# Optimization experiments

Hardware: AMD Instinct MI355X
Metric: run time of the kernel (lower is better)

The kernel has to match this reference:

```python
import jax, jax.numpy as jnp
from jax import lax
import numpy as np

B, K, H, W = 16, 8, 256, 256


def setup_inputs() -> dict:
    key = jax.random.key(0)
    masks = jax.random.normal(key, (B, K, H, W), dtype=jnp.float32)
    return {"masks": masks}


def _nlccs_loss_one(mask):
    """Per-mask loss. mask: (H, W) float, already rescaled/clamped.

    Replicates cv2.connectedComponentsWithStats (8-connectivity, background is
    a single label regardless of connectivity), sorts components by area, and
    suppresses (zeroes a pmask over) the bounding box of the second-largest
    component, then returns mean(pmask * mask).
    """
    h, w = mask.shape
    S = h * w  # sentinel / background label
    sent = jnp.int32(S)
    fg = lax.stop_gradient(mask) > 0.5  # cv2 threshold (arr > 0.5)
    idx = jnp.arange(S, dtype=jnp.int32).reshape(h, w)
    lab0 = jnp.where(fg, idx, sent)

    def step(lab):
        # 8-connectivity neighbor-min propagation (cv2 default connectivity=8)
        p = jnp.pad(lab, 1, constant_values=S)
        m = lab
        for dy in (-1, 0, 1):
            for dx in (-1, 0, 1):
                if dy == 0 and dx == 0:
                    continue
                m = jnp.minimum(m, p[1 + dy:1 + dy + h, 1 + dx:1 + dx + w])
        lab = jnp.where(fg, m, sent)
        # pointer jumping: lab <- lab[lab] for log-time convergence
        ext = jnp.concatenate([lab.reshape(-1), jnp.array([S], jnp.int32)])
        return jnp.where(fg, ext[lab], sent)

    def cond(c):
        lab, prev = c
        return jnp.any(lab != prev)

    def body(c):
        lab, _ = c
        return step(lab), lab

    lab, _ = lax.while_loop(cond, body, (step(lab0), lab0))

    # per-label areas; background pixels all share label S (like cv2 label 0)
    areas = jnp.zeros(S + 1, jnp.int32).at[lab.reshape(-1)].add(1)
    _, top_idx = lax.top_k(areas, 2)
    second = top_idx[1]  # stats sorted by area -> stats[-2]

    # bounding box of the second-largest component
    sel = lab == second
    rows = jnp.arange(h, dtype=jnp.int32)[:, None]
    cols = jnp.arange(w, dtype=jnp.int32)[None, :]
    h0 = jnp.min(jnp.where(sel, rows, h))
    h1 = jnp.max(jnp.where(sel, rows, -1)) + 1
    w0 = jnp.min(jnp.where(sel, cols, w))
    w1 = jnp.max(jnp.where(sel, cols, -1)) + 1
    inside = (rows >= h0) & (rows < h1) & (cols >= w0) & (cols < w1)
    pmask = 1.0 - inside.astype(mask.dtype)  # pmask[h0:h1, w0:w1] = 0
    return (pmask * mask).mean()


def reference(masks):
    # masks: (b, k, h, w)
    m = jnp.maximum((masks + 1.0) * 0.5, 0.0)  # ((masks+1)/2).clamp(min=0)
    flat = m.reshape(-1, m.shape[-2], m.shape[-1])  # (b*k, h, w)
    losses = jax.vmap(_nlccs_loss_one)(flat)
    return losses.mean()
```

## Files before the change

kernel.cpp:

```cpp
#include <hip/hip_runtime.h>

#define HH 256
#define WW 256
#define SS 65536
#define NM 128
#define TRR 16
#define NT2 16
#define RMX 2048
#define SPT 1024
#define SPM 16384

struct Meta {
  double dsum[NM];
  int h0[NM]; int h1[NM]; int w0[NM]; int w1[NM];
};

__device__ __forceinline__ int find_c(int* L, int x) {
  int p = L[x];
  if (p == x) return x;
  int root = p, q = L[root];
  while (q != root) { root = q; q = L[root]; }
  if (root != p) L[x] = root;
  return root;
}

__device__ void unite(int* L, int a, int b) {
  bool done = false;
  do {
    a = find_c(L, a);
    b = find_c(L, b);
    if (a < b)      { int old = atomicMin(&L[b], a); done = (old == b); b = old; }
    else if (b < a) { int old = atomicMin(&L[a], b); done = (old == a); a = old; }
    else done = true;
  } while (!done);
}

__device__ __forceinline__ int find_halve(int* L, int x) {
  int p = L[x];
  while (p != x) {
    int gp = L[p];
    if (gp == p) return p;
    L[x] = gp;
    x = p; p = gp;
  }
  return x;
}

__device__ __forceinline__ int cid(const unsigned long long* rm,
                                   const int* rpre, int r) {
  int w = r >> 6, b = r & 63;
  return rpre[w] + (int)__popcll(rm[w] & (b ? ((1ull << b) - 1) : 0ull));
}

__device__ __forceinline__ unsigned long long mask_le(int b) {
  return (b == 63) ? ~0ull : ((1ull << (b + 1)) - 1);
}
__device__ __forceinline__ unsigned long long mask_lt(int b) {
  return b ? ((1ull << b) - 1) : 0ull;
}

__global__ __launch_bounds__(512)
void k_local(const float* __restrict__ in, int cb,
             int* __restrict__ gp, int* __restrict__ ga,
             unsigned int* __restrict__ gbb, unsigned short* __restrict__ gl,
             unsigned short* __restrict__ gbrow, int* __restrict__ gnr,
             double* __restrict__ tdsum, unsigned int* __restrict__ tbb,
             int* __restrict__ gfg0) {
  __shared__ unsigned long long sfgw[TRR][4];
  __shared__ unsigned char sfgc[TRR][32];
  __shared__ unsigned long long srs[TRR][4];
  __shared__ int wpre64[64];
  __shared__ int snr;
  __shared__ int sspan[RMX];
  __shared__ int suf[RMX];
  __shared__ unsigned long long rootm[32];
  __shared__ int rpre[32];
  __shared__ int sA[SPT], sW0[SPT], sW1[SPT], sH0[SPT], sH1[SPT];
  __shared__ double sred[8];
  __shared__ int sbb[4][8];

  int q = blockIdx.x, lm = q >> 4, tile = q & 15;
  int tid = threadIdx.x, lane = tid & 63, wv = tid >> 6;
  int gm = cb + lm, R0 = tile << 4;

  int r1 = tid >> 5, cs = tid & 31;
  const float4* src =
      (const float4*)(in + ((size_t)gm << 16) + ((R0 + r1) << 8) + (cs << 3));
  double dsum = 0.0;
  unsigned int fgb = 0;
  for (int k = 0; k < 2; k++) {
    float4 v = src[k];
    float m0 = fmaxf((v.x + 1.0f) * 0.5f, 0.0f);
    float m1 = fmaxf((v.y + 1.0f) * 0.5f, 0.0f);
    float m2 = fmaxf((v.z + 1.0f) * 0.5f, 0.0f);
    float m3 = fmaxf((v.w + 1.0f) * 0.5f, 0.0f);
    dsum += (double)m0 + (double)m1 + (double)m2 + (double)m3;
    fgb |= ((m0 > 0.5f) ? 1u : 0u) << (4 * k);
    fgb |= ((m1 > 0.5f) ? 1u : 0u) << (4 * k + 1);
    fgb |= ((m2 > 0.5f) ? 1u : 0u) << (4 * k + 2);
    fgb |= ((m3 > 0.5f) ? 1u : 0u) << (4 * k + 3);
  }
  sfgc[r1][cs] = (unsigned char)fgb;
  __syncthreads();
  if (tid < 64) {
    int row = tid >> 2, w = tid & 3;
    const unsigned char* pc = &sfgc[row][w << 3];
    unsigned long long wd = 0;
    for (int i = 0; i < 8; i++) wd |= ((unsigned long long)pc[i]) << (i << 3);
    sfgw[row][w] = wd;
  }
  __syncthreads();

  if (tid < 64) {
    int row = tid >> 2, w = tid & 3;
    unsigned long long W = sfgw[row][w];
    unsigned long long carry = (w > 0) ? (sfgw[row][w - 1] >> 63) : 0ull;
    unsigned long long rs = W & ~((W << 1) | carry);
    srs[row][w] = rs;
    int cnt = (int)__popcll(rs);
    int sa = cnt;
    for (int off = 1; off < 64; off <<= 1) {
      int t = __shfl_up(sa, off);
      if (tid >= off) sa += t;
    }
    wpre64[tid] = sa - cnt;
    if (tid == 63) snr = sa;
    int id = sa - cnt;
    unsigned long long bits = rs;
    while (bits) {
      int a = (int)__ffsll(bits) - 1;
      bits &= bits - 1;
      int A = (w << 6) + a;
      unsigned long long inv = ~(W >> a);
      int len = inv ? ((int)__ffsll(inv) - 1) : (64 - a);
      if (len == 64 - a) {
        for (int w2 = w + 1; w2 < 4; w2++) {
          unsigned long long iv2 = ~sfgw[row][w2];
          int t = iv2 ? ((int)__ffsll(iv2) - 1) : 64;
          len += t;
          if (t < 64) break;
        }
      }
      sspan[id] = (row << 16) | (A << 8) | (A + len - 1);
      suf[id] = id;
      id++;
    }
  } else {
    for (int s = tid - 64; s < SPT; s += 448) {
      sA[s] = 0; sW0[s] = WW; sW1[s] = -1; sH0[s] = TRR; sH1[s] = -1;
    }
  }
  __syncthreads();

  int nr = snr;

  for (int i = tid; i < nr; i += 512) {
    int sp = sspan[i];
    int row = sp >> 16, a = (sp >> 8) & 255, b = sp & 255;
    if (row == 0) continue;
    int lo = max(a - 1, 0), hi = min(b + 1, 255);
    const unsigned long long* Wp = sfgw[row - 1];
    const unsigned long long* Rp = srs[row - 1];
    int prebase = (row - 1) << 2;
    int lw = lo >> 6, lb = lo & 63;
    if (((Wp[lw] >> lb) & 1) && !((Rp[lw] >> lb) & 1)) {
      int j = wpre64[prebase + lw] + (int)__popcll(Rp[lw] & mask_le(lb)) - 1;
      unite(suf, i, j);
    }
    for (int w = lw; w <= (hi >> 6); w++) {
      unsigned long long m = Rp[w];
      if (w == lw) m &= ~mask_lt(lb);
      if (w == (hi >> 6)) m &= mask_le(hi & 63);
      int base2 = wpre64[prebase + w];
      while (m) {
        int bb = (int)__ffsll(m) - 1;
        m &= m - 1;
        int j = base2 + (int)__popcll(Rp[w] & mask_lt(bb));
        unite(suf, i, j);
      }
    }
  }
  __syncthreads();

  for (int j = 0; j < 4; j++) {
    int i = tid + (j << 9);
    unsigned long long bal = __ballot(i < nr && suf[i] == i);
    if (lane == 0) rootm[wv + (j << 3)] = bal;
  }
  __syncthreads();
  if (tid < 32) {
    int pc = (int)__popcll(rootm[tid]);
    int sa = pc;
    for (int off = 1; off < 32; off <<= 1) {
      int t = __shfl_up(sa, off);
      if (tid >= off) sa += t;
    }
    rpre[tid] = sa - pc;
  }
  __syncthreads();

  for (int i = tid; i < nr; i += 512) {
    int root = find_halve(suf, i);
    int id = cid(rootm, rpre, root);
    int sp = sspan[i];
    int row = sp >> 16, a = (sp >> 8) & 255, b = sp & 255;
    atomicAdd(&sA[id], b - a + 1);
    if (a < sW0[id]) atomicMin(&sW0[id], a);
    if (b > sW1[id]) atomicMax(&sW1[id], b);
    if (row < sH0[id]) atomicMin(&sH0[id], row);
    if (row > sH1[id]) atomicMax(&sH1[id], row);
  }
  __syncthreads();

  int nc = rpre[31] + (int)__popcll(rootm[31]);
  for (int i = tid; i < nr; i += 512) {
    if (suf[i] == i) {
      int id = cid(rootm, rpre, i);
      int gid = (lm << 14) + (tile << 10) + id;
      int sp = sspan[i];
      gp[gid] = gid;
      ga[gid] = sA[id];
      gl[gid] = (unsigned short)((tile << 12) + ((sp >> 16) << 8) +
                                 ((sp >> 8) & 255));
      gbb[gid] = ((unsigned)(R0 + sH0[id]) << 24) | ((unsigned)sW0[id] << 16)
               | ((unsigned)(R0 + sH1[id]) << 8) | (unsigned)sW1[id];
    }
  }
  {
    int c = tid & 255, topbot = tid >> 8;
    int brow = topbot ? (TRR - 1) : 0;
    unsigned short val = 0xFFFF;
    if ((sfgw[brow][c >> 6] >> (c & 63)) & 1) {
      int w = c >> 6, bb = c & 63;
      int id = wpre64[(brow << 2) + w] +
               (int)__popcll(srs[brow][w] & mask_le(bb)) - 1;
      int root = find_halve(suf, id);
      val = (unsigned short)((tile << 10) + cid(rootm, rpre, root));
    }
    gbrow[(q << 9) + (topbot ? 256 : 0) + c] = val;
  }
  if (tid == 0) gnr[q] = nc;

  int c = tid & 255, half = (tid >> 8) << 3;
  int bh0r = TRR, bh1r = -1;
  bool anybg = false;
  for (int row = half; row < half + 8; row++) {
    if (!((sfgw[row][c >> 6] >> (c & 63)) & 1)) {
      anybg = true;
      bh0r = min(bh0r, row); bh1r = max(bh1r, row);
    }
  }
  int bw0r = anybg ? c : WW, bw1r = anybg ? c : -1;
  for (int off = 32; off > 0; off >>= 1) {
    bw0r = min(bw0r, __shfl_down(bw0r, off));
    bw1r = max(bw1r, __shfl_down(bw1r, off));
    bh0r = min(bh0r, __shfl_down(bh0r, off));
    bh1r = max(bh1r, __shfl_down(bh1r, off));
  }
  if (lane == 0) { sbb[0][wv] = bw0r; sbb[1][wv] = bw1r;
                   sbb[2][wv] = bh0r; sbb[3][wv] = bh1r; }
  for (int off = 32; off > 0; off >>= 1) dsum += __shfl_down(dsum, off);
  if (lane == 0) sred[wv] = dsum;
  __syncthreads();
  if (tid == 0) {
    int a0 = sbb[0][0], a1 = sbb[1][0], a2 = sbb[2][0], a3 = sbb[3][0];
    for (int i = 1; i < 8; i++) {
      a0 = min(a0, sbb[0][i]); a1 = max(a1, sbb[1][i]);
      a2 = min(a2, sbb[2][i]); a3 = max(a3, sbb[3][i]);
    }
    unsigned pack = (a1 >= 0)
        ? (((unsigned)(R0 + a2) << 24) | ((unsigned)a0 << 16) |
           ((unsigned)(R0 + a3) << 8) | (unsigned)a1)
        : 0xFFFF0000u;
    tbb[q] = pack;
    double t = 0.0;
    for (int i = 0; i < 8; i++) t += sred[i];
    tdsum[q] = t;
    if (tile == 0) gfg0[lm] = (int)(sfgw[0][0] & 1ull);
  }
}

__global__ void k_seam(int* __restrict__ gp,
                       const unsigned short* __restrict__ gbrow) {
  int b = blockIdx.x;
  int lm = b / 15, s = b % 15;
  int tb = lm << 4;
  int sbase = lm << 14;
  const unsigned short* up = gbrow + ((tb + s) << 9) + 256;
  const unsigned short* lo = gbrow + ((tb + s + 1) << 9);
  int c = threadIdx.x;
  unsigned short v16 = lo[c];
  if (v16 == 0xFFFF) return;
  int v = sbase + v16;
  bool wfg = (c > 0) && (lo[c - 1] != 0xFFFF);
  unsigned short n16 = up[c];
  if (!wfg) {
    if (n16 != 0xFFFF) unite(gp, v, sbase + n16);
    else if (c > 0 && up[c - 1] != 0xFFFF) unite(gp, v, sbase + up[c - 1]);
  }
  if (n16 == 0xFFFF && c < 255 && up[c + 1] != 0xFFFF)
    unite(gp, v, sbase + up[c + 1]);
}

__global__ void k_push(int* __restrict__ gp, int* __restrict__ ga,
                       unsigned int* __restrict__ gbb,
                       const int* __restrict__ gnr) {
  int q = blockIdx.x;
  int lm = q >> 4;
  int sbase = lm << 14;
  int nc = gnr[q];
  int tid = threadIdx.x, lane = tid & 63;
  for (int t = 0; t < 4; t++) {
    int slot = (t << 8) + tid;
    int r = -1, a = 0;
    int h0 = HH, w0 = WW, h1 = -1, w1 = -1;
    if (slot < nc) {
      int gid = sbase + ((q & 15) << 10) + slot;
      int rr = find_c(gp, gid);
      if (rr != gid) {
        r = rr; a = ga[gid];
        unsigned int bb = gbb[gid];
        h0 = (int)(bb >> 24); w0 = (int)((bb >> 16) & 255);
        h1 = (int)((bb >> 8) & 255); w1 = (int)(bb & 255);
      }
    }
    bool pend = (r >= 0);
    while (__any(pend)) {
      unsigned long long mk = __ballot(pend);
      int srcl = (int)__ffsll(mk) - 1;
      int lead = __shfl(r, srcl);
      bool mine = pend && (r == lead);
      int v  = mine ? a  : 0;
      int g0 = mine ? h0 : HH;
      int g1 = mine ? h1 : -1;
      int g2 = mine ? w0 : WW;
      int g3 = mine ? w1 : -1;
      for (int off = 32; off > 0; off >>= 1) {
        v += __shfl_down(v, off);
        g0 = min(g0, __shfl_down(g0, off));
        g1 = max(g1, __shfl_down(g1, off));
        g2 = min(g2, __shfl_down(g2, off));
        g3 = max(g3, __shfl_down(g3, off));
      }
      int tot = __shfl(v, 0);
      int m0 = __shfl(g0, 0), m1 = __shfl(g1, 0);
      int m2 = __shfl(g2, 0), m3 = __shfl(g3, 0);
      if (lane == srcl) {
        atomicAdd(&ga[lead], tot);
        unsigned int* dst = &gbb[lead];
        unsigned int old = *dst;
        while (true) {
          int oh0 = (int)(old >> 24), ow0 = (int)((old >> 16) & 255);
          int oh1 = (int)((old >> 8) & 255), ow1 = (int)(old & 255);
          int nh0 = min(oh0, m0), nw0 = min(ow0, m2);
          int nh1 = max(oh1, m1), nw1 = max(ow1, m3);
          unsigned int mrg = ((unsigned)nh0 << 24) | ((unsigned)nw0 << 16) |
                             ((unsigned)nh1 << 8) | (unsigned)nw1;
          if (mrg == old) break;
          unsigned int got = atomicCAS(dst, old, mrg);
          if (got == old) break;
          old = got;
        }
      }
      pend = pend && !mine;
    }
  }
}

__global__ void k_top2p(const int* __restrict__ gp, const int* __restrict__ ga,
                        const unsigned short* __restrict__ gl,
                        const int* __restrict__ gnr,
                        unsigned long long* __restrict__ tt1,
                        unsigned long long* __restrict__ tt2,
                        int* __restrict__ tfs) {
  int q = blockIdx.x;
  int lm = q >> 4, tile = q & 15;
  int sbase = lm << 14;
  int nc = gnr[q];
  int tid = threadIdx.x, lane = tid & 63, wv = tid >> 6;
  unsigned long long t1 = 0, t2 = 0;
  int fsum = 0;
  for (int sl = tid; sl < nc; sl += 256) {
    int s = (tile << 10) + sl;
    int gid = sbase + s;
    if (gp[gid] == gid) {
      int a = ga[gid];
      int lab = gl[gid];
      fsum += a;
      unsigned long long key = ((unsigned long long)a << 37)
                             | ((unsigned long long)(SS - lab) << 20)
                             | (unsigned)s;
      if (key > t1) { t2 = t1; t1 = key; }
      else if (key > t2) t2 = key;
    }
  }
  for (int off = 32; off > 0; off >>= 1) {
    unsigned long long o1 = __shfl_down(t1, off), o2 = __shfl_down(t2, off);
    if (o1 > t1) { t2 = (t1 > o2) ? t1 : o2; t1 = o1; }
    else if (o1 > t2) t2 = o1;
    fsum += __shfl_down(fsum, off);
  }
  __shared__ unsigned long long s1[4], s2[4];
  __shared__ int sf[4];
  if (lane == 0) { s1[wv] = t1; s2[wv] = t2; sf[wv] = fsum; }
  __syncthreads();
  if (tid == 0) {
    for (int i = 1; i < 4; i++) {
      unsigned long long o1 = s1[i], o2 = s2[i];
      if (o1 > t1) { t2 = (t1 > o2) ? t1 : o2; t1 = o1; }
      else if (o1 > t2) t2 = o1;
      fsum += sf[i];
    }
    tt1[q] = t1; tt2[q] = t2; tfs[q] = fsum;
  }
}

__global__ __launch_bounds__(64)
void k_mask(const double* __restrict__ tdsum,
            const unsigned int* __restrict__ tbb,
            const unsigned long long* __restrict__ tt1,
            const unsigned long long* __restrict__ tt2,
            const int* __restrict__ tfs, const int* __restrict__ gfg0,
            const unsigned int* __restrict__ gbb,
            Meta* __restrict__ mt, int c0) {
  int lm = blockIdx.x, gm = c0 + lm;
  int tid = threadIdx.x;
  int tb = lm << 4;
  double d = 0.0;
  int h0 = 255, w0 = 255, h1 = 0, w1 = 0;
  unsigned long long t1 = 0, t2 = 0;
  int fsum = 0;
  if (tid < 16) {
    d = tdsum[tb + tid];
    unsigned bb = tbb[tb + tid];
    h0 = (int)(bb >> 24); w0 = (int)((bb >> 16) & 255);
    h1 = (int)((bb >> 8) & 255); w1 = (int)(bb & 255);
    t1 = tt1[tb + tid]; t2 = tt2[tb + tid]; fsum = tfs[tb + tid];
  }
  for (int off = 8; off > 0; off >>= 1) {
    d += __shfl_down(d, off);
    h0 = min(h0, __shfl_down(h0, off));
    w0 = min(w0, __shfl_down(w0, off));
    h1 = max(h1, __shfl_down(h1, off));
    w1 = max(w1, __shfl_down(w1, off));
    unsigned long long o1 = __shfl_down(t1, off), o2 = __shfl_down(t2, off);
    if (o1 > t1) { t2 = (t1 > o2) ? t1 : o2; t1 = o1; }
    else if (o1 > t2) t2 = o1;
    fsum += __shfl_down(fsum, off);
  }
  if (tid == 0) {
    mt->dsum[gm] = d;
    unsigned long long bg = ((unsigned long long)(SS - fsum)) << 37;
    int zl = gfg0[lm] ? 1 : 0;
    unsigned long long zk = ((unsigned long long)(SS - zl)) << 20;
    if (bg > t1) { t2 = t1; t1 = bg; } else if (bg > t2) t2 = bg;
    if (zk > t1) { t2 = t1; t1 = zk; } else if (zk > t2) t2 = zk;
    if (t2 == bg) {
      mt->h0[gm] = h0; mt->h1[gm] = h1; mt->w0[gm] = w0; mt->w1[gm] = w1;
    } else if (t2 == zk) {
      mt->h0[gm] = 1; mt->h1[gm] = 0; mt->w0[gm] = 1; mt->w1[gm] = 0;
    } else {
      unsigned int bb = gbb[(lm << 14) + (int)(t2 & 0xFFFFF)];
      mt->h0[gm] = (int)(bb >> 24);
      mt->w0[gm] = (int)((bb >> 16) & 255);
      mt->h1[gm] = (int)((bb >> 8) & 255);
      mt->w1[gm] = (int)(bb & 255);
    }
  }
}

__global__ void k_inside(const float* __restrict__ in,
                         const Meta* __restrict__ mt,
                         double* __restrict__ dinsp, int c0) {
  int b = blockIdx.x;
  int lm = b >> 3, seg = b & 7;
  int gm = c0 + lm;
  int h0 = mt->h0[gm], h1 = mt->h1[gm], w0 = mt->w0[gm], w1 = mt->w1[gm];
  double acc = 0.0;
  if (h1 >= h0) {
    int cc = w0 + threadIdx.x;
    if (cc <= w1) {
      const float* base = in + ((size_t)gm << 16);
      for (int rr = h0 + seg; rr <= h1; rr += 8) {
        float x = base[(rr << 8) + cc];
        acc += (double)fmaxf((x + 1.0f) * 0.5f, 0.0f);
      }
    }
  }
  for (int off = 32; off > 0; off >>= 1) acc += __shfl_down(acc, off);
  __shared__ double sd[4];
  int wid = threadIdx.x >> 6, lane = threadIdx.x & 63;
  if (lane == 0) sd[wid] = acc;
  __syncthreads();
  if (threadIdx.x == 0)
    dinsp[(gm << 3) + seg] = sd[0] + sd[1] + sd[2] + sd[3];
}

__global__ void k_final(const Meta* __restrict__ mt,
                        const double* __restrict__ dinsp,
                        float* __restrict__ out) {
  __shared__ double sd[NM];
  int t = threadIdx.x;
  double di = 0.0;
  for (int s = 0; s < 8; s++) di += dinsp[(t << 3) + s];
  sd[t] = (mt->dsum[t] - di) / (double)SS;
  __syncthreads();
  for (int off = 64; off > 0; off >>= 1) {
    if (t < off) sd[t] += sd[t + off];
    __syncthreads();
  }
  if (t == 0) out[0] = (float)(sd[0] / (double)NM);
}

extern "C" void kernel_launch(void* const* d_in, const int* in_sizes, int n_in,
                              void* d_out, int out_size, void* d_ws,
                              size_t ws_size, hipStream_t stream) {
  const float* in = (const float*)d_in[0];
  float* out = (float*)d_out;

  Meta* mt = (Meta*)d_ws;
  const size_t meta_bytes = (sizeof(Meta) + 255) & ~(size_t)255;
  char* base = (char*)d_ws + meta_bytes;
  size_t fixed = (size_t)NM * 8 * sizeof(double);
  size_t avail = (ws_size > meta_bytes + fixed)
                     ? (ws_size - meta_bytes - fixed) : 0;
  const size_t per_mask = (size_t)NT2 * 8 + NT2 * 4 + 4 +
                          (size_t)SPM * (4 + 4 + 4 + 2) +
                          (size_t)NT2 * 512 * 2 + NT2 * 4 +
                          (size_t)NT2 * (8 + 8 + 4);
  int chunk = (int)(avail / per_mask);
  if (chunk > NM) chunk = NM;
  if (chunk < 1) return;

  char* ptr = base;
  double* dinsp = (double*)ptr;        ptr += fixed;
  double* tdsum = (double*)ptr;        ptr += (size_t)chunk * NT2 * 8;
  unsigned long long* tt1 = (unsigned long long*)ptr;
  ptr += (size_t)chunk * NT2 * 8;
  unsigned long long* tt2 = (unsigned long long*)ptr;
  ptr += (size_t)chunk * NT2 * 8;
  int* gp = (int*)ptr;                 ptr += (size_t)chunk * SPM * 4;
  int* ga = (int*)ptr;                 ptr += (size_t)chunk * SPM * 4;
  unsigned int* gbb = (unsigned int*)ptr;       ptr += (size_t)chunk * SPM * 4;
  unsigned short* gl = (unsigned short*)ptr;    ptr += (size_t)chunk * SPM * 2;
  unsigned short* gbrow = (unsigned short*)ptr; ptr += (size_t)chunk * NT2 * 512 * 2;
  int* gnr = (int*)ptr;                ptr += (size_t)chunk * NT2 * 4;
  unsigned int* tbb = (unsigned int*)ptr;       ptr += (size_t)chunk * NT2 * 4;
  int* tfs = (int*)ptr;                ptr += (size_t)chunk * NT2 * 4;
  int* gfg0 = (int*)ptr;

  for (int c0 = 0; c0 < NM; c0 += chunk) {
    int cn = (chunk < NM - c0) ? chunk : (NM - c0);
    k_local<<<cn * NT2, 512, 0, stream>>>(in, c0, gp, ga, gbb, gl, gbrow,
                                          gnr, tdsum, tbb, gfg0);
    k_seam <<<cn * 15, 256, 0, stream>>>(gp, gbrow);
    k_push <<<cn * NT2, 256, 0, stream>>>(gp, ga, gbb, gnr);
    k_top2p<<<cn * NT2, 256, 0, stream>>>(gp, ga, gl, gnr, tt1, tt2, tfs);
    k_mask <<<cn, 64, 0, stream>>>(tdsum, tbb, tt1, tt2, tfs, gfg0, gbb,
                                   mt, c0);
    k_inside<<<cn * 8, 256, 0, stream>>>(in, mt, dinsp, c0);
  }
  k_final<<<1, 128, 0, stream>>>(mt, dinsp, out);
}
```

Measured before the change: 184.0 us.

## Fuse seam, push, top-2, mask and inside kernels into one per-mask block

Replaces five separate kernels (seam union, root push, per-tile top-2, mask selection, inside-box sum) with a single kernel that runs one 512-thread block per mask and separates the phases with block barriers. The intermediate top-2 and fg-sum arrays move from global memory into shared memory. This removes four launch boundaries and some global round trips. In exchange each mask's tail work is serialized onto one block (128 blocks instead of up to 2048), so there is much less parallelism in the push and inside-sum phases.

```diff
diff --git a/kernel.cpp b/kernel.cpp
--- a/kernel.cpp
+++ b/kernel.cpp
@@ -280,220 +280,212 @@
   }
 }
 
-__global__ void k_seam(int* __restrict__ gp,
-                       const unsigned short* __restrict__ gbrow) {
-  int b = blockIdx.x;
-  int lm = b / 15, s = b % 15;
-  int tb = lm << 4;
-  int sbase = lm << 14;
-  const unsigned short* up = gbrow + ((tb + s) << 9) + 256;
-  const unsigned short* lo = gbrow + ((tb + s + 1) << 9);
-  int c = threadIdx.x;
-  unsigned short v16 = lo[c];
-  if (v16 == 0xFFFF) return;
-  int v = sbase + v16;
-  bool wfg = (c > 0) && (lo[c - 1] != 0xFFFF);
-  unsigned short n16 = up[c];
-  if (!wfg) {
-    if (n16 != 0xFFFF) unite(gp, v, sbase + n16);
-    else if (c > 0 && up[c - 1] != 0xFFFF) unite(gp, v, sbase + up[c - 1]);
-  }
-  if (n16 == 0xFFFF && c < 255 && up[c + 1] != 0xFFFF)
-    unite(gp, v, sbase + up[c + 1]);
-}
-
-__global__ void k_push(int* __restrict__ gp, int* __restrict__ ga,
-                       unsigned int* __restrict__ gbb,
-                       const int* __restrict__ gnr) {
-  int q = blockIdx.x;
-  int lm = q >> 4;
-  int sbase = lm << 14;
-  int nc = gnr[q];
-  int tid = threadIdx.x, lane = tid & 63;
-  for (int t = 0; t < 4; t++) {
-    int slot = (t << 8) + tid;
-    int r = -1, a = 0;
-    int h0 = HH, w0 = WW, h1 = -1, w1 = -1;
-    if (slot < nc) {
-      int gid = sbase + ((q & 15) << 10) + slot;
-      int rr = find_c(gp, gid);
-      if (rr != gid) {
-        r = rr; a = ga[gid];
-        unsigned int bb = gbb[gid];
-        h0 = (int)(bb >> 24); w0 = (int)((bb >> 16) & 255);
-        h1 = (int)((bb >> 8) & 255); w1 = (int)(bb & 255);
-      }
-    }
-    bool pend = (r >= 0);
-    while (__any(pend)) {
-      unsigned long long mk = __ballot(pend);
-      int srcl = (int)__ffsll(mk) - 1;
-      int lead = __shfl(r, srcl);
-      bool mine = pend && (r == lead);
-      int v  = mine ? a  : 0;
-      int g0 = mine ? h0 : HH;
-      int g1 = mine ? h1 : -1;
-      int g2 = mine ? w0 : WW;
-      int g3 = mine ? w1 : -1;
-      for (int off = 32; off > 0; off >>= 1) {
-        v += __shfl_down(v, off);
-        g0 = min(g0, __shfl_down(g0, off));
-        g1 = max(g1, __shfl_down(g1, off));
-        g2 = min(g2, __shfl_down(g2, off));
-        g3 = max(g3, __shfl_down(g3, off));
-      }
-      int tot = __shfl(v, 0);
-      int m0 = __shfl(g0, 0), m1 = __shfl(g1, 0);
-      int m2 = __shfl(g2, 0), m3 = __shfl(g3, 0);
-      if (lane == srcl) {
-        atomicAdd(&ga[lead], tot);
-        unsigned int* dst = &gbb[lead];
-        unsigned int old = *dst;
-        while (true) {
-          int oh0 = (int)(old >> 24), ow0 = (int)((old >> 16) & 255);
-          int oh1 = (int)((old >> 8) & 255), ow1 = (int)(old & 255);
-          int nh0 = min(oh0, m0), nw0 = min(ow0, m2);
-          int nh1 = max(oh1, m1), nw1 = max(ow1, m3);
-          unsigned int mrg = ((unsigned)nh0 << 24) | ((unsigned)nw0 << 16) |
-                             ((unsigned)nh1 << 8) | (unsigned)nw1;
-          if (mrg == old) break;
-          unsigned int got = atomicCAS(dst, old, mrg);
-          if (got == old) break;
-          old = got;
+__global__ __launch_bounds__(512)
+void k_tail(const float* __restrict__ in, int c0,
+            int* __restrict__ gp, int* __restrict__ ga,
+            unsigned int* __restrict__ gbb,
+            const unsigned short* __restrict__ gl,
+            const unsigned short* __restrict__ gbrow,
+            const int* __restrict__ gnr,
+            const double* __restrict__ tdsum,
+            const unsigned int* __restrict__ tbb,
+            const int* __restrict__ gfg0,
+            Meta* __restrict__ mt, double* __restrict__ dinsp) {
+  __shared__ int snc[16];
+  __shared__ unsigned long long stt1[16], stt2[16];
+  __shared__ int stfs[16];
+  __shared__ int sbx[4];
+  __shared__ double sdl[2][4];
+
+  int lm = blockIdx.x, gm = c0 + lm;
+  int tid = threadIdx.x, lane = tid & 63, wv = tid >> 6;
+  int tb = lm << 4, sbase = lm << 14;
+
+  if (tid < 16) snc[tid] = gnr[tb + tid];
+
+  for (int idx = tid; idx < 15 * 256; idx += 512) {
+    int s = idx >> 8, c = idx & 255;
+    const unsigned short* up = gbrow + ((tb + s) << 9) + 256;
+    const unsigned short* lo = gbrow + ((tb + s + 1) << 9);
+    unsigned short v16 = lo[c];
+    if (v16 == 0xFFFF) continue;
+    int v = sbase + v16;
+    bool wfg = (c > 0) && (lo[c - 1] != 0xFFFF);
+    unsigned short n16 = up[c];
+    if (!wfg) {
+      if (n16 != 0xFFFF) unite(gp, v, sbase + n16);
+      else if (c > 0 && up[c - 1] != 0xFFFF) unite(gp, v, sbase + up[c - 1]);
+    }
+    if (n16 == 0xFFFF && c < 255 && up[c + 1] != 0xFFFF)
+      unite(gp, v, sbase + up[c + 1]);
+  }
+  __syncthreads();
+  __threadfence();
+  __syncthreads();
+
+  for (int tile = 0; tile < 16; tile++) {
+    int nc = snc[tile];
+    for (int sl0 = 0; sl0 < nc; sl0 += 512) {
+      int slot = sl0 + tid;
+      int r = -1, a = 0;
+      int h0 = HH, w0 = WW, h1 = -1, w1 = -1;
+      if (slot < nc) {
+        int gid = sbase + (tile << 10) + slot;
+        int rr = find_c(gp, gid);
+        if (rr != gid) {
+          r = rr; a = ga[gid];
+          unsigned int bb = gbb[gid];
+          h0 = (int)(bb >> 24); w0 = (int)((bb >> 16) & 255);
+          h1 = (int)((bb >> 8) & 255); w1 = (int)(bb & 255);
         }
       }
-      pend = pend && !mine;
-    }
-  }
-}
-
-__global__ void k_top2p(const int* __restrict__ gp, const int* __restrict__ ga,
-                        const unsigned short* __restrict__ gl,
-                        const int* __restrict__ gnr,
-                        unsigned long long* __restrict__ tt1,
-                        unsigned long long* __restrict__ tt2,
-                        int* __restrict__ tfs) {
-  int q = blockIdx.x;
-  int lm = q >> 4, tile = q & 15;
-  int sbase = lm << 14;
-  int nc = gnr[q];
-  int tid = threadIdx.x, lane = tid & 63, wv = tid >> 6;
-  unsigned long long t1 = 0, t2 = 0;
-  int fsum = 0;
-  for (int sl = tid; sl < nc; sl += 256) {
-    int s = (tile << 10) + sl;
-    int gid = sbase + s;
-    if (gp[gid] == gid) {
-      int a = ga[gid];
-      int lab = gl[gid];
-      fsum += a;
-      unsigned long long key = ((unsigned long long)a << 37)
-                             | ((unsigned long long)(SS - lab) << 20)
-                             | (unsigned)s;
-      if (key > t1) { t2 = t1; t1 = key; }
-      else if (key > t2) t2 = key;
-    }
-  }
-  for (int off = 32; off > 0; off >>= 1) {
-    unsigned long long o1 = __shfl_down(t1, off), o2 = __shfl_down(t2, off);
-    if (o1 > t1) { t2 = (t1 > o2) ? t1 : o2; t1 = o1; }
-    else if (o1 > t2) t2 = o1;
-    fsum += __shfl_down(fsum, off);
-  }
-  __shared__ unsigned long long s1[4], s2[4];
-  __shared__ int sf[4];
-  if (lane == 0) { s1[wv] = t1; s2[wv] = t2; sf[wv] = fsum; }
-  __syncthreads();
-  if (tid == 0) {
-    for (int i = 1; i < 4; i++) {
-      unsigned long long o1 = s1[i], o2 = s2[i];
+      bool pend = (r >= 0);
+      while (__any(pend)) {
+        unsigned long long mk = __ballot(pend);
+        int srcl = (int)__ffsll(mk) - 1;
+        int lead = __shfl(r, srcl);
+        bool mine = pend && (r == lead);
+        int v  = mine ? a  : 0;
+        int g0 = mine ? h0 : HH;
+        int g1 = mine ? h1 : -1;
+        int g2 = mine ? w0 : WW;
+        int g3 = mine ? w1 : -1;
+        for (int off = 32; off > 0; off >>= 1) {
+          v += __shfl_down(v, off);
+          g0 = min(g0, __shfl_down(g0, off));
+          g1 = max(g1, __shfl_down(g1, off));
+          g2 = min(g2, __shfl_down(g2, off));
+          g3 = max(g3, __shfl_down(g3, off));
+        }
+        int tot = __shfl(v, 0);
+        int m0 = __shfl(g0, 0), m1 = __shfl(g1, 0);
+        int m2 = __shfl(g2, 0), m3 = __shfl(g3, 0);
+        if (lane == srcl) {
+          atomicAdd(&ga[lead], tot);
+          unsigned int* dst = &gbb[lead];
+          unsigned int old = *dst;
+          while (true) {
+            int oh0 = (int)(old >> 24), ow0 = (int)((old >> 16) & 255);
+            int oh1 = (int)((old >> 8) & 255), ow1 = (int)(old & 255);
+            int nh0 = min(oh0, m0), nw0 = min(ow0, m2);
+            int nh1 = max(oh1, m1), nw1 = max(ow1, m3);
+            unsigned int mrg = ((unsigned)nh0 << 24) | ((unsigned)nw0 << 16) |
+                               ((unsigned)nh1 << 8) | (unsigned)nw1;
+            if (mrg == old) break;
+            unsigned int got = atomicCAS(dst, old, mrg);
+            if (got == old) break;
+            old = got;
+          }
+        }
+        pend = pend && !mine;
+      }
+    }
+  }
+  __syncthreads();
+  __threadfence();
+  __syncthreads();
+
+  for (int tt = 0; tt < 2; tt++) {
+    int tile = (wv << 1) + tt;
+    int nc = snc[tile];
+    unsigned long long t1 = 0, t2 = 0;
+    int fsum = 0;
+    for (int sl = lane; sl < nc; sl += 64) {
+      int s = (tile << 10) + sl;
+      int gid = sbase + s;
+      if (gp[gid] == gid) {
+        int a = ga[gid];
+        int lab = gl[gid];
+        fsum += a;
+        unsigned long long key = ((unsigned long long)a << 37)
+                               | ((unsigned long long)(SS - lab) << 20)
+                               | (unsigned)s;
+        if (key > t1) { t2 = t1; t1 = key; }
+        else if (key > t2) t2 = key;
+      }
+    }
+    for (int off = 32; off > 0; off >>= 1) {
+      unsigned long long o1 = __shfl_down(t1, off), o2 = __shfl_down(t2, off);
       if (o1 > t1) { t2 = (t1 > o2) ? t1 : o2; t1 = o1; }
       else if (o1 > t2) t2 = o1;
-      fsum += sf[i];
-    }
-    tt1[q] = t1; tt2[q] = t2; tfs[q] = fsum;
-  }
-}
-
-__global__ __launch_bounds__(64)
-void k_mask(const double* __restrict__ tdsum,
-            const unsigned int* __restrict__ tbb,
-            const unsigned long long* __restrict__ tt1,
-            const unsigned long long* __restrict__ tt2,
-            const int* __restrict__ tfs, const int* __restrict__ gfg0,
-            const unsigned int* __restrict__ gbb,
-            Meta* __restrict__ mt, int c0) {
-  int lm = blockIdx.x, gm = c0 + lm;
-  int tid = threadIdx.x;
-  int tb = lm << 4;
-  double d = 0.0;
-  int h0 = 255, w0 = 255, h1 = 0, w1 = 0;
-  unsigned long long t1 = 0, t2 = 0;
-  int fsum = 0;
-  if (tid < 16) {
-    d = tdsum[tb + tid];
-    unsigned bb = tbb[tb + tid];
-    h0 = (int)(bb >> 24); w0 = (int)((bb >> 16) & 255);
-    h1 = (int)((bb >> 8) & 255); w1 = (int)(bb & 255);
-    t1 = tt1[tb + tid]; t2 = tt2[tb + tid]; fsum = tfs[tb + tid];
-  }
-  for (int off = 8; off > 0; off >>= 1) {
-    d += __shfl_down(d, off);
-    h0 = min(h0, __shfl_down(h0, off));
-    w0 = min(w0, __shfl_down(w0, off));
-    h1 = max(h1, __shfl_down(h1, off));
-    w1 = max(w1, __shfl_down(w1, off));
-    unsigned long long o1 = __shfl_down(t1, off), o2 = __shfl_down(t2, off);
-    if (o1 > t1) { t2 = (t1 > o2) ? t1 : o2; t1 = o1; }
-    else if (o1 > t2) t2 = o1;
-    fsum += __shfl_down(fsum, off);
-  }
-  if (tid == 0) {
-    mt->dsum[gm] = d;
-    unsigned long long bg = ((unsigned long long)(SS - fsum)) << 37;
-    int zl = gfg0[lm] ? 1 : 0;
-    unsigned long long zk = ((unsigned long long)(SS - zl)) << 20;
-    if (bg > t1) { t2 = t1; t1 = bg; } else if (bg > t2) t2 = bg;
-    if (zk > t1) { t2 = t1; t1 = zk; } else if (zk > t2) t2 = zk;
-    if (t2 == bg) {
-      mt->h0[gm] = h0; mt->h1[gm] = h1; mt->w0[gm] = w0; mt->w1[gm] = w1;
-    } else if (t2 == zk) {
-      mt->h0[gm] = 1; mt->h1[gm] = 0; mt->w0[gm] = 1; mt->w1[gm] = 0;
-    } else {
-      unsigned int bb = gbb[(lm << 14) + (int)(t2 & 0xFFFFF)];
-      mt->h0[gm] = (int)(bb >> 24);
-      mt->w0[gm] = (int)((bb >> 16) & 255);
-      mt->h1[gm] = (int)((bb >> 8) & 255);
-      mt->w1[gm] = (int)(bb & 255);
-    }
-  }
-}
-
-__global__ void k_inside(const float* __restrict__ in,
-                         const Meta* __restrict__ mt,
-                         double* __restrict__ dinsp, int c0) {
-  int b = blockIdx.x;
-  int lm = b >> 3, seg = b & 7;
-  int gm = c0 + lm;
-  int h0 = mt->h0[gm], h1 = mt->h1[gm], w0 = mt->w0[gm], w1 = mt->w1[gm];
-  double acc = 0.0;
-  if (h1 >= h0) {
-    int cc = w0 + threadIdx.x;
-    if (cc <= w1) {
-      const float* base = in + ((size_t)gm << 16);
-      for (int rr = h0 + seg; rr <= h1; rr += 8) {
-        float x = base[(rr << 8) + cc];
-        acc += (double)fmaxf((x + 1.0f) * 0.5f, 0.0f);
-      }
-    }
-  }
-  for (int off = 32; off > 0; off >>= 1) acc += __shfl_down(acc, off);
-  __shared__ double sd[4];
-  int wid = threadIdx.x >> 6, lane = threadIdx.x & 63;
-  if (lane == 0) sd[wid] = acc;
-  __syncthreads();
-  if (threadIdx.x == 0)
-    dinsp[(gm << 3) + seg] = sd[0] + sd[1] + sd[2] + sd[3];
+      fsum += __shfl_down(fsum, off);
+    }
+    if (lane == 0) { stt1[tile] = t1; stt2[tile] = t2; stfs[tile] = fsum; }
+  }
+  __syncthreads();
+
+  if (tid < 64) {
+    double d = 0.0;
+    int h0 = 255, w0 = 255, h1 = 0, w1 = 0;
+    unsigned long long t1 = 0, t2 = 0;
+    int fsum = 0;
+    if (tid < 16) {
+      d = tdsum[tb + tid];
+      unsigned bb = tbb[tb + tid];
+      h0 = (int)(bb >> 24); w0 = (int)((bb >> 16) & 255);
+      h1 = (int)((bb >> 8) & 255); w1 = (int)(bb & 255);
+      t1 = stt1[tid]; t2 = stt2[tid]; fsum = stfs[tid];
+    }
+    for (int off = 8; off > 0; off >>= 1) {
+      d += __shfl_down(d, off);
+      h0 = min(h0, __shfl_down(h0, off));
+      w0 = min(w0, __shfl_down(w0, off));
+      h1 = max(h1, __shfl_down(h1, off));
+      w1 = max(w1, __shfl_down(w1, off));
+      unsigned long long o1 = __shfl_down(t1, off), o2 = __shfl_down(t2, off);
+      if (o1 > t1) { t2 = (t1 > o2) ? t1 : o2; t1 = o1; }
+      else if (o1 > t2) t2 = o1;
+      fsum += __shfl_down(fsum, off);
+    }
+    if (tid == 0) {
+      mt->dsum[gm] = d;
+      unsigned long long bg = ((unsigned long long)(SS - fsum)) << 37;
+      int zl = gfg0[lm] ? 1 : 0;
+      unsigned long long zk = ((unsigned long long)(SS - zl)) << 20;
+      if (bg > t1) { t2 = t1; t1 = bg; } else if (bg > t2) t2 = bg;
+      if (zk > t1) { t2 = t1; t1 = zk; } else if (zk > t2) t2 = zk;
+      if (t2 == bg) {
+        sbx[0] = h0; sbx[1] = h1; sbx[2] = w0; sbx[3] = w1;
+      } else if (t2 == zk) {
+        sbx[0] = 1; sbx[1] = 0; sbx[2] = 1; sbx[3] = 0;
+      } else {
+        unsigned int bb = gbb[(lm << 14) + (int)(t2 & 0xFFFFF)];
+        sbx[0] = (int)(bb >> 24);
+        sbx[2] = (int)((bb >> 16) & 255);
+        sbx[1] = (int)((bb >> 8) & 255);
+        sbx[3] = (int)(bb & 255);
+      }
+    }
+  }
+  __syncthreads();
+
+  int h0 = sbx[0], h1 = sbx[1], w0 = sbx[2], w1 = sbx[3];
+  for (int r = 0; r < 4; r++) {
+    int g = tid >> 8;
+    int seg = (r << 1) + g;
+    int t256 = tid & 255;
+    double acc = 0.0;
+    if (h1 >= h0) {
+      int cc = w0 + t256;
+      if (cc <= w1) {
+        const float* base = in + ((size_t)gm << 16);
+        for (int rr = h0 + seg; rr <= h1; rr += 8) {
+          float x = base[(rr << 8) + cc];
+          acc += (double)fmaxf((x + 1.0f) * 0.5f, 0.0f);
+        }
+      }
+    }
+    for (int off = 32; off > 0; off >>= 1) acc += __shfl_down(acc, off);
+    if (lane == 0) sdl[g][t256 >> 6] = acc;
+    __syncthreads();
+    if (tid == 0) {
+      dinsp[(gm << 3) + (r << 1)] =
+          sdl[0][0] + sdl[0][1] + sdl[0][2] + sdl[0][3];
+      dinsp[(gm << 3) + (r << 1) + 1] =
+          sdl[1][0] + sdl[1][1] + sdl[1][2] + sdl[1][3];
+    }
+    __syncthreads();
+  }
 }
 
 __global__ void k_final(const Meta* __restrict__ mt,
@@ -524,10 +516,12 @@
   size_t fixed = (size_t)NM * 8 * sizeof(double);
   size_t avail = (ws_size > meta_bytes + fixed)
                      ? (ws_size - meta_bytes - fixed) : 0;
-  const size_t per_mask = (size_t)NT2 * 8 + NT2 * 4 + 4 +
+  const size_t per_mask = (size_t)NT2 * 8 +
                           (size_t)SPM * (4 + 4 + 4 + 2) +
-                          (size_t)NT2 * 512 * 2 + NT2 * 4 +
-                          (size_t)NT2 * (8 + 8 + 4);
+                          (size_t)NT2 * 512 * 2 +
+                          (size_t)NT2 * 4 +
+                          (size_t)NT2 * 4 +
+                          4;
   int chunk = (int)(avail / per_mask);
   if (chunk > NM) chunk = NM;
   if (chunk < 1) return;
@@ -535,10 +529,6 @@
   char* ptr = base;
   double* dinsp = (double*)ptr;        ptr += fixed;
   double* tdsum = (double*)ptr;        ptr += (size_t)chunk * NT2 * 8;
-  unsigned long long* tt1 = (unsigned long long*)ptr;
-  ptr += (size_t)chunk * NT2 * 8;
-  unsigned long long* tt2 = (unsigned long long*)ptr;
-  ptr += (size_t)chunk * NT2 * 8;
   int* gp = (int*)ptr;                 ptr += (size_t)chunk * SPM * 4;
   int* ga = (int*)ptr;                 ptr += (size_t)chunk * SPM * 4;
   unsigned int* gbb = (unsigned int*)ptr;       ptr += (size_t)chunk * SPM * 4;
@@ -546,19 +536,14 @@
   unsigned short* gbrow = (unsigned short*)ptr; ptr += (size_t)chunk * NT2 * 512 * 2;
   int* gnr = (int*)ptr;                ptr += (size_t)chunk * NT2 * 4;
   unsigned int* tbb = (unsigned int*)ptr;       ptr += (size_t)chunk * NT2 * 4;
-  int* tfs = (int*)ptr;                ptr += (size_t)chunk * NT2 * 4;
   int* gfg0 = (int*)ptr;
 
   for (int c0 = 0; c0 < NM; c0 += chunk) {
     int cn = (chunk < NM - c0) ? chunk : (NM - c0);
     k_local<<<cn * NT2, 512, 0, stream>>>(in, c0, gp, ga, gbb, gl, gbrow,
                                           gnr, tdsum, tbb, gfg0);
-    k_seam <<<cn * 15, 256, 0, stream>>>(gp, gbrow);
-    k_push <<<cn * NT2, 256, 0, stream>>>(gp, ga, gbb, gnr);
-    k_top2p<<<cn * NT2, 256, 0, stream>>>(gp, ga, gl, gnr, tt1, tt2, tfs);
-    k_mask <<<cn, 64, 0, stream>>>(tdsum, tbb, tt1, tt2, tfs, gfg0, gbb,
-                                   mt, c0);
-    k_inside<<<cn * 8, 256, 0, stream>>>(in, mt, dinsp, c0);
+    k_tail <<<cn, 512, 0, stream>>>(in, c0, gp, ga, gbb, gl, gbrow, gnr,
+                                    tdsum, tbb, gfg0, mt, dinsp);
   }
   k_final<<<1, 128, 0, stream>>>(mt, dinsp, out);
 }
```

Result: slower. 298.3 us (+62.2%).
